# Kernel optimization log

Hardware: AMD Instinct MI355X
Metric: run time of the kernel (lower is better)

## Reference

```python
import jax, jax.numpy as jnp
import numpy as np

N_NODES = 100000
N_EDGES = 1600000
MOTIF_DIM = 32
HIDDEN = 64


def setup_inputs() -> dict:
    key = jax.random.key(0)
    k1, k2, k3, k4 = jax.random.split(key, 4)
    motif_x = jax.random.normal(k1, (N_NODES, MOTIF_DIM), dtype=jnp.float32)
    edge_index = jax.random.randint(k2, (2, N_EDGES), 0, N_NODES, dtype=jnp.int64)
    in_dim = 4 * MOTIF_DIM
    W1 = jax.random.normal(k3, (in_dim, HIDDEN), dtype=jnp.float32) / np.sqrt(in_dim)
    b1 = jnp.zeros((HIDDEN,), dtype=jnp.float32)
    W2 = jax.random.normal(k4, (HIDDEN, 1), dtype=jnp.float32) / np.sqrt(HIDDEN)
    b2 = jnp.zeros((1,), dtype=jnp.float32)
    return {"motif_x": motif_x, "edge_index": edge_index, "W1": W1, "b1": b1, "W2": W2, "b2": b2}


def reference(motif_x, edge_index, W1, b1, W2, b2):
    src = edge_index[0]
    dst = edge_index[1]
    mu = motif_x[src]                      # [E, D] gather
    mv = motif_x[dst]                      # [E, D] gather
    feats = jnp.concatenate([mu, mv, jnp.abs(mu - mv), mu * mv], axis=1)  # [E, 4D]
    h = jax.nn.relu(feats @ W1 + b1)       # [E, H]
    g = jax.nn.sigmoid(h @ W2 + b2)[:, 0]  # [E]
    return jnp.clip(g, 0.0, 1.0)
```

## Files before the change

### kernel.cpp

```cpp
#include <hip/hip_runtime.h>

#define D 32
#define H 64

typedef __attribute__((ext_vector_type(8))) short bf16x8;
typedef __attribute__((ext_vector_type(4))) float f32x4;

union AB { uint4 u; bf16x8 v; };

__device__ __forceinline__ short f2bf_s(float f) {
  unsigned u = __float_as_uint(f);
  u += 0x7fffu + ((u >> 16) & 1u);
  return (short)(u >> 16);
}

__device__ __forceinline__ unsigned pack_bf2(float lo, float hi) {
  return __builtin_amdgcn_perm(__float_as_uint(hi), __float_as_uint(lo), 0x07060302u);
}

__global__ __launch_bounds__(256) void prep(
    const float* __restrict__ x, const float* __restrict__ W1,
    short* __restrict__ xbf, short* __restrict__ btab, int n4, int nPack) {
  int b = blockIdx.x;
  if (b < nPack) {
    int i = b * 256 + threadIdx.x;
    if (i < n4) {
      float4 v = ((const float4*)x)[i];
      short4 o;
      o.x = f2bf_s(v.x); o.y = f2bf_s(v.y); o.z = f2bf_s(v.z); o.w = f2bf_s(v.w);
      ((short4*)xbf)[i] = o;
    }
  } else {
    int id = (b - nPack) * 256 + threadIdx.x;
    if (id < 16 * 64 * 8) {
      int j = id & 7;
      int l = (id >> 3) & 63;
      int f = id >> 9;
      int s = f & 3, t = f >> 2;
      int k = s * 32 + (l >> 4) * 8 + j;
      int n = t * 16 + (l & 15);
      btab[id] = f2bf_s(W1[k * H + n]);
    }
  }
}

__device__ __forceinline__ void compute_tile(
    uint4 muU, uint4 mvU, const bf16x8* __restrict__ B,
    const float* __restrict__ b1v, const float* __restrict__ w2v, float bias2,
    int tile, int q, int m, int nE, float* __restrict__ out) {
  AB mu, mv, ac, ap;
  mu.u = muU; mv.u = mvU;
#pragma unroll
  for (int k = 0; k < 4; ++k) {
    unsigned a = (&mu.u.x)[k], b = (&mv.u.x)[k];
    float alo = __uint_as_float(a << 16);
    float ahi = __uint_as_float(a & 0xffff0000u);
    float blo = __uint_as_float(b << 16);
    float bhi = __uint_as_float(b & 0xffff0000u);
    float dlo = alo - blo, dhi = ahi - bhi;
    (&ac.u.x)[k] = pack_bf2(dlo, dhi) & 0x7fff7fffu;
    (&ap.u.x)[k] = pack_bf2(alo * blo, ahi * bhi);
  }

  float part[4];
#pragma unroll
  for (int t = 0; t < 4; ++t) {
    float bv = b1v[t];
    f32x4 acc = (f32x4){bv, bv, bv, bv};
    acc = __builtin_amdgcn_mfma_f32_16x16x32_bf16(mu.v, B[t * 4 + 0], acc, 0, 0, 0);
    acc = __builtin_amdgcn_mfma_f32_16x16x32_bf16(mv.v, B[t * 4 + 1], acc, 0, 0, 0);
    acc = __builtin_amdgcn_mfma_f32_16x16x32_bf16(ac.v, B[t * 4 + 2], acc, 0, 0, 0);
    acc = __builtin_amdgcn_mfma_f32_16x16x32_bf16(ap.v, B[t * 4 + 3], acc, 0, 0, 0);
#pragma unroll
    for (int r = 0; r < 4; ++r) {
      float h = fmaxf(acc[r], 0.f);
      part[r] = (t == 0) ? h * w2v[0] : fmaf(h, w2v[t], part[r]);
    }
  }

#pragma unroll
  for (int mask = 1; mask < 16; mask <<= 1)
#pragma unroll
    for (int r = 0; r < 4; ++r)
      part[r] += __shfl_xor(part[r], mask, 64);

  if (m < 4) {
    int ew = tile * 16 + q * 4 + m;
    if (ew < nE) {
      float z = part[m] + bias2;
      out[ew] = 1.f / (1.f + __expf(-z));
    }
  }
}

__global__ __launch_bounds__(256) void edge_mfma(
    const short* __restrict__ xbf, const short* __restrict__ btab,
    const int* __restrict__ ei,
    const float* __restrict__ b1, const float* __restrict__ W2,
    const float* __restrict__ b2, float* __restrict__ out,
    int nE, int nTiles) {
  int lane = threadIdx.x & 63;
  int wid  = (blockIdx.x * 256 + threadIdx.x) >> 6;
  int nW   = (gridDim.x * 256) >> 6;
  int m = lane & 15;
  int q = lane >> 4;
  int nChunks = (nTiles + 3) >> 2;
  if (wid >= nChunks) return;

  bf16x8 B[16];
#pragma unroll
  for (int f = 0; f < 16; ++f)
    B[f] = *(const bf16x8*)(btab + (f * 64 + lane) * 8);

  float b1v[4], w2v[4];
#pragma unroll
  for (int t = 0; t < 4; ++t) {
    b1v[t] = b1[t * 16 + m];
    w2v[t] = W2[t * 16 + m];
  }
  float bias2 = b2[0];

  const uint4* xb = (const uint4*)xbf;
  int eLim = nE - 1;
  int cLim = nChunks - 1;

  int sn[4], dn[4], s2[4], d2[4];
  uint4 amu[4], amv[4];

  int c = wid;
#pragma unroll
  for (int t = 0; t < 4; ++t) {
    int e = c * 64 + t * 16 + m; e = e < nE ? e : eLim;
    sn[t] = ei[e]; dn[t] = ei[e + nE];
  }
#pragma unroll
  for (int t = 0; t < 4; ++t) {
    amu[t] = xb[sn[t] * 4 + q];
    amv[t] = xb[dn[t] * 4 + q];
  }
  {
    int cc = c + nW; cc = cc < nChunks ? cc : cLim;
#pragma unroll
    for (int t = 0; t < 4; ++t) {
      int e = cc * 64 + t * 16 + m; e = e < nE ? e : eLim;
      sn[t] = ei[e]; dn[t] = ei[e + nE];
    }
  }

  while (c < nChunks) {
    int cn = c + nW;
    {
      int cc = cn + nW; cc = cc < nChunks ? cc : cLim;
#pragma unroll
      for (int t = 0; t < 4; ++t) {
        int e = cc * 64 + t * 16 + m; e = e < nE ? e : eLim;
        s2[t] = ei[e]; d2[t] = ei[e + nE];
      }
    }
#pragma unroll
    for (int t = 0; t < 4; ++t) {
      compute_tile(amu[t].x == 0xFFFFFFFFu && amu[t].y == 0xFFFFFFFFu ? amu[t] : amu[t],
                   amv[t], B, b1v, w2v, bias2, c * 4 + t, q, m, nE, out);
      amu[t] = xb[sn[t] * 4 + q];
      amv[t] = xb[dn[t] * 4 + q];
    }
#pragma unroll
    for (int t = 0; t < 4; ++t) { sn[t] = s2[t]; dn[t] = d2[t]; }
    c = cn;
  }
}

__global__ __launch_bounds__(256) void edge_full(
    const float* __restrict__ x, const int* __restrict__ ei,
    const float* __restrict__ W1, const float* __restrict__ b1,
    const float* __restrict__ W2, const float* __restrict__ b2,
    float* __restrict__ out, int nE) {
  int e = blockIdx.x * 256 + threadIdx.x;
  if (e >= nE) return;
  int s = ei[e];
  int d = ei[e + nE];
  const float4* mu4 = (const float4*)(x + (size_t)s * D);
  const float4* mv4 = (const float4*)(x + (size_t)d * D);
  float mu[D], mv[D], c[D], p[D];
#pragma unroll
  for (int qq = 0; qq < D / 4; ++qq) {
    float4 a = mu4[qq];
    float4 b = mv4[qq];
    mu[4*qq+0] = a.x; mv[4*qq+0] = b.x; c[4*qq+0] = fabsf(a.x-b.x); p[4*qq+0] = a.x*b.x;
    mu[4*qq+1] = a.y; mv[4*qq+1] = b.y; c[4*qq+1] = fabsf(a.y-b.y); p[4*qq+1] = a.y*b.y;
    mu[4*qq+2] = a.z; mv[4*qq+2] = b.z; c[4*qq+2] = fabsf(a.z-b.z); p[4*qq+2] = a.z*b.z;
    mu[4*qq+3] = a.w; mv[4*qq+3] = b.w; c[4*qq+3] = fabsf(a.w-b.w); p[4*qq+3] = a.w*b.w;
  }
  float z = b2[0];
  for (int j = 0; j < H; ++j) {
    float a = b1[j];
#pragma unroll
    for (int k = 0; k < D; ++k) {
      a = fmaf(mu[k], W1[k * H + j], a);
      a = fmaf(mv[k], W1[(D + k) * H + j], a);
      a = fmaf(c[k],  W1[(2 * D + k) * H + j], a);
      a = fmaf(p[k],  W1[(3 * D + k) * H + j], a);
    }
    a = fmaxf(a, 0.f);
    z = fmaf(a, W2[j], z);
  }
  float g = 1.f / (1.f + __expf(-z));
  out[e] = fminf(fmaxf(g, 0.f), 1.f);
}

extern "C" void kernel_launch(void* const* d_in, const int* in_sizes, int n_in,
                              void* d_out, int out_size, void* d_ws, size_t ws_size,
                              hipStream_t stream) {
  const float* x  = (const float*)d_in[0];
  const int*   ei = (const int*)d_in[1];
  const float* W1 = (const float*)d_in[2];
  const float* b1 = (const float*)d_in[3];
  const float* W2 = (const float*)d_in[4];
  const float* b2 = (const float*)d_in[5];
  float* out = (float*)d_out;

  int nN = in_sizes[0] / D;
  int nE = in_sizes[1] / 2;

  size_t xbf_shorts = (size_t)nN * D;
  size_t need = (xbf_shorts + 16 * 64 * 8) * sizeof(short);
  if (ws_size >= need) {
    short* xbf  = (short*)d_ws;
    short* btab = xbf + xbf_shorts;
    int n4 = nN * D / 4;
    int nPack = (n4 + 255) / 256;
    int nBt = (16 * 64 * 8 + 255) / 256;
    prep<<<nPack + nBt, 256, 0, stream>>>(x, W1, xbf, btab, n4, nPack);
    int nTiles = (nE + 15) / 16;
    edge_mfma<<<2048, 256, 0, stream>>>(xbf, btab, ei, b1, W2, b2, out, nE, nTiles);
  } else {
    edge_full<<<(nE + 255) / 256, 256, 0, stream>>>(x, ei, W1, b1, W2, b2, out, nE);
  }
}
```

Before: 130.8 us.

## Use DPP row reductions and shuffle-distributed indices with 2-tile pipelined chunks

Replaces the shfl_xor butterfly reduction with DPP row-local adds, which avoid LDS-backed permutes. Each wave now handles 32-edge pairs instead of 64-edge chunks. It loads src/dst indices with a single coalesced load per lane and broadcasts them with __shfl, cutting index-load instructions and registers. Gathers for the next pair are issued before computing the current pair, and launch_bounds adds an occupancy hint. The trade-offs are a shallower prefetch depth and the extra shuffles.

```diff
diff --git a/kernel.cpp b/kernel.cpp
--- a/kernel.cpp
+++ b/kernel.cpp
@@ -16,6 +16,19 @@
 
 __device__ __forceinline__ unsigned pack_bf2(float lo, float hi) {
   return __builtin_amdgcn_perm(__float_as_uint(hi), __float_as_uint(lo), 0x07060302u);
+}
+
+template <int CTRL>
+__device__ __forceinline__ float dppadd(float x) {
+  int s = __builtin_amdgcn_update_dpp(0, __float_as_int(x), CTRL, 0xF, 0xF, true);
+  return x + __int_as_float(s);
+}
+__device__ __forceinline__ float row16_sum(float x) {
+  x = dppadd<0xB1>(x);
+  x = dppadd<0x4E>(x);
+  x = dppadd<0x141>(x);
+  x = dppadd<0x140>(x);
+  return x;
 }
 
 __global__ __launch_bounds__(256) void prep(
@@ -79,33 +92,30 @@
   }
 
 #pragma unroll
-  for (int mask = 1; mask < 16; mask <<= 1)
-#pragma unroll
-    for (int r = 0; r < 4; ++r)
-      part[r] += __shfl_xor(part[r], mask, 64);
+  for (int r = 0; r < 4; ++r) part[r] = row16_sum(part[r]);
 
   if (m < 4) {
     int ew = tile * 16 + q * 4 + m;
     if (ew < nE) {
-      float z = part[m] + bias2;
+      float z = (m == 0 ? part[0] : m == 1 ? part[1] : m == 2 ? part[2] : part[3])
+                + bias2;
       out[ew] = 1.f / (1.f + __expf(-z));
     }
   }
 }
 
-__global__ __launch_bounds__(256) void edge_mfma(
+__global__ __launch_bounds__(256, 4) void edge_mfma(
     const short* __restrict__ xbf, const short* __restrict__ btab,
     const int* __restrict__ ei,
     const float* __restrict__ b1, const float* __restrict__ W2,
     const float* __restrict__ b2, float* __restrict__ out,
-    int nE, int nTiles) {
+    int nE, int nPairs) {
   int lane = threadIdx.x & 63;
   int wid  = (blockIdx.x * 256 + threadIdx.x) >> 6;
   int nW   = (gridDim.x * 256) >> 6;
   int m = lane & 15;
   int q = lane >> 4;
-  int nChunks = (nTiles + 3) >> 2;
-  if (wid >= nChunks) return;
+  if (wid >= nPairs) return;
 
   bf16x8 B[16];
 #pragma unroll
@@ -122,51 +132,45 @@
 
   const uint4* xb = (const uint4*)xbf;
   int eLim = nE - 1;
-  int cLim = nChunks - 1;
-
-  int sn[4], dn[4], s2[4], d2[4];
-  uint4 amu[4], amv[4];
-
-  int c = wid;
-#pragma unroll
-  for (int t = 0; t < 4; ++t) {
-    int e = c * 64 + t * 16 + m; e = e < nE ? e : eLim;
-    sn[t] = ei[e]; dn[t] = ei[e + nE];
-  }
-#pragma unroll
-  for (int t = 0; t < 4; ++t) {
-    amu[t] = xb[sn[t] * 4 + q];
-    amv[t] = xb[dn[t] * 4 + q];
-  }
+  int pLim = nPairs - 1;
+  int selOff = (lane >> 5) ? nE : 0;
+  int eoff = lane & 31;
+
+  int p = wid;
+  int idxNxt;
+  uint4 amu0, amv0, amu1, amv1;
   {
-    int cc = c + nW; cc = cc < nChunks ? cc : cLim;
-#pragma unroll
-    for (int t = 0; t < 4; ++t) {
-      int e = cc * 64 + t * 16 + m; e = e < nE ? e : eLim;
-      sn[t] = ei[e]; dn[t] = ei[e + nE];
-    }
-  }
-
-  while (c < nChunks) {
-    int cn = c + nW;
+    int e = p * 32 + eoff; e = e < nE ? e : eLim;
+    int idxCur = ei[selOff + e];
+    int sn0 = __shfl(idxCur, m);
+    int sn1 = __shfl(idxCur, 16 + m);
+    int dn0 = __shfl(idxCur, 32 + m);
+    int dn1 = __shfl(idxCur, 48 + m);
+    amu0 = xb[sn0 * 4 + q]; amv0 = xb[dn0 * 4 + q];
+    amu1 = xb[sn1 * 4 + q]; amv1 = xb[dn1 * 4 + q];
+    int p1 = p + nW; p1 = p1 < nPairs ? p1 : pLim;
+    int e1 = p1 * 32 + eoff; e1 = e1 < nE ? e1 : eLim;
+    idxNxt = ei[selOff + e1];
+  }
+
+  while (p < nPairs) {
+    int pn = p + nW;
+    int sn0 = __shfl(idxNxt, m);
+    int sn1 = __shfl(idxNxt, 16 + m);
+    int dn0 = __shfl(idxNxt, 32 + m);
+    int dn1 = __shfl(idxNxt, 48 + m);
+    uint4 bmu0 = xb[sn0 * 4 + q], bmv0 = xb[dn0 * 4 + q];
+    uint4 bmu1 = xb[sn1 * 4 + q], bmv1 = xb[dn1 * 4 + q];
     {
-      int cc = cn + nW; cc = cc < nChunks ? cc : cLim;
-#pragma unroll
-      for (int t = 0; t < 4; ++t) {
-        int e = cc * 64 + t * 16 + m; e = e < nE ? e : eLim;
-        s2[t] = ei[e]; d2[t] = ei[e + nE];
-      }
-    }
-#pragma unroll
-    for (int t = 0; t < 4; ++t) {
-      compute_tile(amu[t].x == 0xFFFFFFFFu && amu[t].y == 0xFFFFFFFFu ? amu[t] : amu[t],
-                   amv[t], B, b1v, w2v, bias2, c * 4 + t, q, m, nE, out);
-      amu[t] = xb[sn[t] * 4 + q];
-      amv[t] = xb[dn[t] * 4 + q];
-    }
-#pragma unroll
-    for (int t = 0; t < 4; ++t) { sn[t] = s2[t]; dn[t] = d2[t]; }
-    c = cn;
+      int p2 = pn + nW; p2 = p2 < nPairs ? p2 : pLim;
+      int e2 = p2 * 32 + eoff; e2 = e2 < nE ? e2 : eLim;
+      idxNxt = ei[selOff + e2];
+    }
+    compute_tile(amu0, amv0, B, b1v, w2v, bias2, p * 2,     q, m, nE, out);
+    compute_tile(amu1, amv1, B, b1v, w2v, bias2, p * 2 + 1, q, m, nE, out);
+
+    amu0 = bmu0; amv0 = bmv0; amu1 = bmu1; amv1 = bmv1;
+    p = pn;
   }
 }
 
@@ -232,7 +236,8 @@
     int nBt = (16 * 64 * 8 + 255) / 256;
     prep<<<nPack + nBt, 256, 0, stream>>>(x, W1, xbf, btab, n4, nPack);
     int nTiles = (nE + 15) / 16;
-    edge_mfma<<<2048, 256, 0, stream>>>(xbf, btab, ei, b1, W2, b2, out, nE, nTiles);
+    int nPairs = (nTiles + 1) / 2;
+    edge_mfma<<<2048, 256, 0, stream>>>(xbf, btab, ei, b1, W2, b2, out, nE, nPairs);
   } else {
     edge_full<<<(nE + 255) / 256, 256, 0, stream>>>(x, ei, W1, b1, W2, b2, out, nE);
   }
```

New measurement: 180.2 us. +37.8%, slower.
